# Optimization experiments

Hardware: AMD Instinct MI355X
Metric: run time of the kernel (lower is better)

## Reference

```python
import jax, jax.numpy as jnp
import numpy as np


def setup_inputs() -> dict:
    key = jax.random.key(0)
    ks = jax.random.split(key, 8)
    B, T, V, D, H, C = 1024, 80, 50000, 300, 300, 3
    sent = jax.random.randint(ks[0], (B, T), 0, V, dtype=jnp.int32)
    lens = jax.random.randint(ks[1], (B,), 1, T + 1, dtype=jnp.int32)
    emb = jax.random.normal(ks[2], (V, D), dtype=jnp.float32) * 0.1
    Wx = jax.random.normal(ks[3], (D, 4 * H), dtype=jnp.float32) * 0.05
    Wh = jax.random.normal(ks[4], (H, 4 * H), dtype=jnp.float32) * 0.05
    b = jnp.zeros((4 * H,), dtype=jnp.float32)
    Wout = jax.random.normal(ks[5], (H, C), dtype=jnp.float32) * 0.05
    bout = jnp.zeros((C,), dtype=jnp.float32)
    return {"sent": sent, "lens": lens, "emb": emb, "Wx": Wx, "Wh": Wh,
            "b": b, "Wout": Wout, "bout": bout}


def _lstm_masked(x, mask, Wx, Wh, b, H):
    # x: [B, T, D], mask: [B, T] float. Scan over time keeping h,c in carry.
    B = x.shape[0]
    h0 = jnp.zeros((B, H), dtype=x.dtype)
    c0 = jnp.zeros((B, H), dtype=x.dtype)

    def step(carry, inp):
        h, c = carry
        xt, mt = inp                      # xt: [B, D], mt: [B]
        gates = xt @ Wx + h @ Wh + b      # [B, 4H]
        i, f, g, o = jnp.split(gates, 4, axis=-1)
        i, f, o = jax.nn.sigmoid(i), jax.nn.sigmoid(f), jax.nn.sigmoid(o)
        g = jnp.tanh(g)
        c_new = f * c + i * g
        h_new = o * jnp.tanh(c_new)
        m = mt[:, None]
        h = m * h_new + (1.0 - m) * h     # mask-based state blending
        c = m * c_new + (1.0 - m) * c
        return (h, c), None

    xs = (jnp.swapaxes(x, 0, 1), jnp.swapaxes(mask, 0, 1))  # time-major
    (h, c), _ = jax.lax.scan(step, (h0, c0), xs)
    return h


def reference(sent, lens, emb, Wx, Wh, b, Wout, bout):
    T = sent.shape[1]
    H = Wh.shape[0]
    x = emb[sent]                                         # [B, T, D]
    mask = (jnp.arange(T)[None, :] < lens[:, None]).astype(x.dtype)  # [B, T]
    h = _lstm_masked(x, mask, Wx, Wh, b, H)
    logit = h @ Wout + bout                               # [B, C]
    return logit
```

## Files before the change

### kernel.cpp

```cpp
#include <hip/hip_runtime.h>
#include <hip/hip_fp16.h>


typedef float    f32x4 __attribute__((ext_vector_type(4)));
typedef _Float16 f16;
typedef _Float16 f16x8 __attribute__((ext_vector_type(8)));
typedef unsigned long long u64;

#define NB    1024
#define TT    80
#define NV    50000
#define ND    300
#define KP    320
#define NKT   10
#define SL    75
#define SLP   80
#define NTPG  5
#define NTIL  20
#define TPB   256
#define GRID  256
#define NSLAB 8

#define TAGMASK 0x0001000100010001ULL

#define OFF_EMB   0
#define OFF_WHP   32000000
#define OFF_WXP   32819200
#define OFF_HBUF  33638400
#define HBUF_SZ   (NB * KP)
#define OFF_HF32  38881280
#define WS_NEED   40110080

__global__ __launch_bounds__(256) void absa_prep_emb(
    const float* __restrict__ emb, f16* __restrict__ embb) {
  int i = blockIdx.x * 256 + threadIdx.x;
  if (i >= NV * KP / 8) return;
  int flat = i * 8;
  int row  = flat / KP;
  int k    = flat - row * KP;
  f16x8 o;
  if (k + 7 < ND) {
    float4 a = *reinterpret_cast<const float4*>(emb + row * ND + k);
    float4 b = *reinterpret_cast<const float4*>(emb + row * ND + k + 4);
    o[0] = (f16)a.x; o[1] = (f16)a.y; o[2] = (f16)a.z; o[3] = (f16)a.w;
    o[4] = (f16)b.x; o[5] = (f16)b.y; o[6] = (f16)b.z; o[7] = (f16)b.w;
  } else {
#pragma unroll
    for (int e = 0; e < 8; ++e) {
      int kk = k + e;
      float v = (kk < ND) ? emb[row * ND + kk] : (kk == ND ? 1.0f : 0.0f);
      o[e] = (f16)v;
    }
  }
  *reinterpret_cast<f16x8*>(embb + flat) = o;
}

__global__ __launch_bounds__(256) void absa_prep_pack2(
    const float* __restrict__ Wx, const float* __restrict__ Wh,
    const float* __restrict__ bias,
    f16* __restrict__ wxp, f16* __restrict__ whp) {
  const int half = 4 * NTIL * NKT * 512;
  int idx0 = blockIdx.x * 256 + threadIdx.x;
  if (idx0 >= 2 * half) return;
  int mode = idx0 >= half;
  int idx  = idx0 - mode * half;
  int e    = idx & 7;
  int lane = (idx >> 3) & 63;
  int fid  = idx >> 9;
  int kt   = fid % NKT;
  int rem  = fid / NKT;
  int nt   = rem % NTIL;
  int n    = rem / NTIL;
  int gi   = nt / NTPG, ti = nt - gi * NTPG;
  int k    = kt * 32 + (lane >> 4) * 8 + e;
  int cc   = ti * 16 + (lane & 15);
  float v = 0.f;
  if (cc < SL) {
    int col = gi * 300 + n * SL + cc;
    if (mode == 0) {
      if (k < ND)       v = Wx[k * 1200 + col];
      else if (k == ND) v = bias[col];
    } else {
      int kl = k % SLP, n2 = k / SLP;
      if (kl < SL)      v = Wh[(n2 * SL + kl) * 1200 + col];
    }
  }
  (mode ? whp : wxp)[idx] = (f16)v;
}

__device__ __forceinline__ float sigf(float x) {
  return __builtin_amdgcn_rcpf(1.f + __builtin_amdgcn_exp2f(-1.44269504f * x));
}
__device__ __forceinline__ float tanhf_(float x) {
  float xx = fminf(15.f, fmaxf(-15.f, x));
  return 1.f - 2.f * __builtin_amdgcn_rcpf(1.f + __builtin_amdgcn_exp2f(2.88539008f * xx));
}

__device__ __forceinline__ u64 tag_pat(int tg) {
  return ((u64)(tg & 1)) | ((u64)((tg >> 1) & 1) << 16) |
         ((u64)((tg >> 2) & 1) << 32) | ((u64)((tg >> 3) & 1) << 48);
}

__global__ __launch_bounds__(TPB, 1) void absa_lstm(
    const int* __restrict__ sent, const int* __restrict__ lens,
    const f16* __restrict__ embb,
    const f16* __restrict__ whp, const f16* __restrict__ wxp,
    f16* __restrict__ hbuf, float* __restrict__ hf32) {
  const int bid = blockIdx.x;
  const int s   = bid & 7;
  const int q   = bid >> 3;
  const int n   = q & 3;
  const int g   = s * 8 + (q >> 2);

  const int tid = threadIdx.x;
  const int w   = tid >> 6;
  const int l   = tid & 63;
  const int l15 = l & 15, lk = l >> 4;
  const int grow0 = g * 16;

  __shared__ float gates[2 * 4 * 80 * 20];
  __shared__ float c_lds[80 * 20];
  __shared__ float hf_lds[80 * 20];
  __shared__ int   sent_lds[16 * TT];
  __shared__ int   len_lds[16];

  for (int i = tid; i < 16 * TT; i += TPB) sent_lds[i] = sent[g * 16 * TT + i];
  if (tid < 16) len_lds[tid] = lens[grow0 + tid];
  for (int i = tid; i < 80 * 20; i += TPB) { c_lds[i] = 0.f; hf_lds[i] = 0.f; }
  __syncthreads();

  int maxlen = 0;
#pragma unroll
  for (int r = 0; r < 16; ++r) maxlen = max(maxlen, len_lds[r]);

  f16x8 wh[NTPG][NKT], wx[NTPG][NKT];
#pragma unroll
  for (int j = 0; j < NTPG; ++j)
#pragma unroll
    for (int kt = 0; kt < NKT; ++kt) {
      size_t off = ((size_t)(n * NTIL + (w * NTPG + j)) * NKT + kt) * 512 + l * 8;
      wh[j][kt] = *reinterpret_cast<const f16x8*>(whp + off);
      wx[j][kt] = *reinterpret_cast<const f16x8*>(wxp + off);
    }

  int gaddr[NTPG];
#pragma unroll
  for (int j = 0; j < NTPG; ++j)
    gaddr[j] = ((w * 80) + j * 16 + l15) * 20 + lk * 4;

  f32x4 acc[NTPG];

  auto xpart = [&](int t) {
#pragma unroll
    for (int j = 0; j < NTPG; ++j) acc[j] = (f32x4){0.f, 0.f, 0.f, 0.f};
    const int srow = sent_lds[l15 * TT + t];
    const f16* xb = embb + (size_t)srow * KP + lk * 8;
#pragma unroll
    for (int kt = 0; kt < NKT; ++kt) {
      f16x8 xa = *reinterpret_cast<const f16x8*>(xb + kt * 32);
#pragma unroll
      for (int j = 0; j < NTPG; ++j)
        acc[j] = __builtin_amdgcn_mfma_f32_16x16x32_f16(xa, wx[j][kt], acc[j], 0, 0, 0);
    }
  };

  xpart(0);

  for (int t = 0; t < maxlen; ++t) {
    const int par = (t & 1) * (4 * 80 * 20);

    if (t > 0) {
      const u64 expv = tag_pat((t - 1) % 15);
      const f16* hp = hbuf + (size_t)((t - 1) & 7) * HBUF_SZ + (grow0 + l15) * KP + lk * 8;
      u64 q0[NKT], q1[NKT];
#pragma unroll
      for (int kt = 0; kt < NKT; ++kt) {
        const u64* p = reinterpret_cast<const u64*>(hp + kt * 32);
        q0[kt] = __hip_atomic_load(p,     __ATOMIC_RELAXED, __HIP_MEMORY_SCOPE_AGENT);
        q1[kt] = __hip_atomic_load(p + 1, __ATOMIC_RELAXED, __HIP_MEMORY_SCOPE_AGENT);
      }
      bool any = true;
      int guard = 0;
      while (any && guard++ < (1 << 15)) {
        any = false;
#pragma unroll
        for (int kt = 0; kt < NKT; ++kt) {
          const u64* p = reinterpret_cast<const u64*>(hp + kt * 32);
          if ((q0[kt] & TAGMASK) != expv) {
            q0[kt] = __hip_atomic_load(p,     __ATOMIC_RELAXED, __HIP_MEMORY_SCOPE_AGENT);
            any = true;
          }
          if ((q1[kt] & TAGMASK) != expv) {
            q1[kt] = __hip_atomic_load(p + 1, __ATOMIC_RELAXED, __HIP_MEMORY_SCOPE_AGENT);
            any = true;
          }
        }
      }
#pragma unroll
      for (int kt = 0; kt < NKT; ++kt) {
        union { u64 qq[2]; f16x8 v; } u;
        u.qq[0] = q0[kt]; u.qq[1] = q1[kt];
#pragma unroll
        for (int j = 0; j < NTPG; ++j)
          acc[j] = __builtin_amdgcn_mfma_f32_16x16x32_f16(u.v, wh[j][kt], acc[j], 0, 0, 0);
      }
    }

#pragma unroll
    for (int j = 0; j < NTPG; ++j)
      *reinterpret_cast<f32x4*>(&gates[par + gaddr[j]]) = acc[j];
    __syncthreads();

    {
      const u64 pat = tag_pat(t % 15);
      f16* hc = hbuf + (size_t)(t & 7) * HBUF_SZ;
      for (int i = tid; i < 320; i += TPB) {
        int row = i & 15, qd = i >> 4;
        union { unsigned short us[4]; u64 uu; } pu;
#pragma unroll
        for (int e = 0; e < 4; ++e) {
          int cc = qd * 4 + e;
          float h = 0.f;
          if (cc < SL) {
            int base = cc * 20 + row;
            if (t < len_lds[row]) {
              float vi = gates[par + (0 * 80 + cc) * 20 + row];
              float vf = gates[par + (1 * 80 + cc) * 20 + row];
              float vg = gates[par + (2 * 80 + cc) * 20 + row];
              float vo = gates[par + (3 * 80 + cc) * 20 + row];
              float iv = sigf(vi), fv = sigf(vf), ov = sigf(vo);
              float gv = tanhf_(vg);
              float cn = fv * c_lds[base] + iv * gv;
              h = ov * tanhf_(cn);
              c_lds[base] = cn;
              hf_lds[base] = h;
            } else {
              h = hf_lds[base];
            }
          }
          union { f16 f; unsigned short u; } cv;
          cv.f = (f16)h;
          pu.us[e] = cv.u;
        }
        pu.uu = (pu.uu & ~TAGMASK) | pat;
        u64* dst = reinterpret_cast<u64*>(hc + (size_t)(grow0 + row) * KP + n * SLP + qd * 4);
        (void)__hip_atomic_exchange(dst, pu.uu, __ATOMIC_RELAXED, __HIP_MEMORY_SCOPE_AGENT);
      }
    }

    if (t + 1 < maxlen) xpart(t + 1);
  }

  __syncthreads();
  for (int i = tid; i < 16 * SL; i += TPB) {
    int row = i & 15, cc = i >> 4;
    hf32[(grow0 + row) * ND + n * SL + cc] = hf_lds[cc * 20 + row];
  }
}

__global__ __launch_bounds__(256) void absa_logits(
    const float* __restrict__ hf32, const float* __restrict__ Wout,
    const float* __restrict__ bout, float* __restrict__ out) {
  int row = blockIdx.x * 4 + (threadIdx.x >> 6);
  int l   = threadIdx.x & 63;
  float s0 = 0.f, s1 = 0.f, s2 = 0.f;
  for (int k = l; k < ND; k += 64) {
    float h  = hf32[row * ND + k];
    s0 += h * Wout[k * 3 + 0];
    s1 += h * Wout[k * 3 + 1];
    s2 += h * Wout[k * 3 + 2];
  }
#pragma unroll
  for (int o = 32; o; o >>= 1) {
    s0 += __shfl_down(s0, o);
    s1 += __shfl_down(s1, o);
    s2 += __shfl_down(s2, o);
  }
  if (l == 0) {
    out[row * 3 + 0] = s0 + bout[0];
    out[row * 3 + 1] = s1 + bout[1];
    out[row * 3 + 2] = s2 + bout[2];
  }
}

extern "C" void kernel_launch(void* const* d_in, const int* in_sizes, int n_in,
                              void* d_out, int out_size, void* d_ws, size_t ws_size,
                              hipStream_t stream) {
  const int*   sent = (const int*)d_in[0];
  const int*   lens = (const int*)d_in[1];
  const float* emb  = (const float*)d_in[2];
  const float* Wx   = (const float*)d_in[3];
  const float* Wh   = (const float*)d_in[4];
  const float* bv   = (const float*)d_in[5];
  const float* Wout = (const float*)d_in[6];
  const float* bout = (const float*)d_in[7];
  float* out = (float*)d_out;

  char* wsb = (char*)d_ws;
  f16*   embb = (f16*)(wsb + OFF_EMB);
  f16*   whp  = (f16*)(wsb + OFF_WHP);
  f16*   wxp  = (f16*)(wsb + OFF_WXP);
  f16*   hbuf = (f16*)(wsb + OFF_HBUF);
  float* hf32 = (float*)(wsb + OFF_HF32);

  (void)hipMemsetAsync(hbuf, 0xFF, NSLAB * NB * KP * 2, stream);

  absa_prep_emb  <<<(NV * KP / 8 + 255) / 256, 256, 0, stream>>>(emb, embb);
  absa_prep_pack2<<<2 * 4 * NTIL * NKT * 512 / 256, 256, 0, stream>>>(Wx, Wh, bv, wxp, whp);
  absa_lstm      <<<GRID, TPB, 0, stream>>>(sent, lens, embb, whp, wxp, hbuf, hf32);
  absa_logits    <<<NB / 4, 256, 0, stream>>>(hf32, Wout, bout, out);
}
```

Baseline: 685.5 us.

## Split LSTM recurrent GEMM K dimension across two wave groups per block

Doubles the block to 512 threads and splits the K dimension of the hidden-state and input matmuls across two groups of four waves. Each group writes its partial gate sums to a separate half of the gates buffer, and the elementwise pass adds the two halves. Each wave now keeps only half of the Wh fragments in registers. Wx is no longer held in registers and is reloaded from global memory on every step. The aim is to shorten each wave's serial MFMA chain and its polling of hbuf. The cost is more global traffic for Wx and a doubled gates buffer in LDS.

```diff
diff --git a/kernel.cpp b/kernel.cpp
--- a/kernel.cpp
+++ b/kernel.cpp
@@ -13,11 +13,12 @@
 #define ND    300
 #define KP    320
 #define NKT   10
+#define KTH   5
 #define SL    75
 #define SLP   80
 #define NTPG  5
 #define NTIL  20
-#define TPB   256
+#define TPB   512
 #define GRID  256
 #define NSLAB 8
 
@@ -101,24 +102,29 @@
          ((u64)((tg >> 2) & 1) << 32) | ((u64)((tg >> 3) & 1) << 48);
 }
 
-__global__ __launch_bounds__(TPB, 1) void absa_lstm(
+#define GSTRIDE (2 * 4 * 80 * 20)
+
+__global__ __launch_bounds__(TPB, 2) void absa_lstm(
     const int* __restrict__ sent, const int* __restrict__ lens,
     const f16* __restrict__ embb,
     const f16* __restrict__ whp, const f16* __restrict__ wxp,
     f16* __restrict__ hbuf, float* __restrict__ hf32) {
   const int bid = blockIdx.x;
   const int s   = bid & 7;
-  const int q   = bid >> 3;
-  const int n   = q & 3;
-  const int g   = s * 8 + (q >> 2);
-
-  const int tid = threadIdx.x;
-  const int w   = tid >> 6;
-  const int l   = tid & 63;
-  const int l15 = l & 15, lk = l >> 4;
+  const int qq  = bid >> 3;
+  const int n   = qq & 3;
+  const int g   = s * 8 + (qq >> 2);
+
+  const int tid  = threadIdx.x;
+  const int w    = tid >> 6;
+  const int gate = w & 3;
+  const int kh   = w >> 2;
+  const int kb   = kh * KTH;
+  const int l    = tid & 63;
+  const int l15  = l & 15, lk = l >> 4;
   const int grow0 = g * 16;
 
-  __shared__ float gates[2 * 4 * 80 * 20];
+  __shared__ float gates[2 * GSTRIDE];
   __shared__ float c_lds[80 * 20];
   __shared__ float hf_lds[80 * 20];
   __shared__ int   sent_lds[16 * TT];
@@ -133,20 +139,18 @@
 #pragma unroll
   for (int r = 0; r < 16; ++r) maxlen = max(maxlen, len_lds[r]);
 
-  f16x8 wh[NTPG][NKT], wx[NTPG][NKT];
+  f16x8 wh[NTPG][KTH];
 #pragma unroll
   for (int j = 0; j < NTPG; ++j)
 #pragma unroll
-    for (int kt = 0; kt < NKT; ++kt) {
-      size_t off = ((size_t)(n * NTIL + (w * NTPG + j)) * NKT + kt) * 512 + l * 8;
-      wh[j][kt] = *reinterpret_cast<const f16x8*>(whp + off);
-      wx[j][kt] = *reinterpret_cast<const f16x8*>(wxp + off);
-    }
+    for (int kk = 0; kk < KTH; ++kk)
+      wh[j][kk] = *reinterpret_cast<const f16x8*>(
+          whp + ((size_t)(n * NTIL + (gate * NTPG + j)) * NKT + (kb + kk)) * 512 + l * 8);
 
   int gaddr[NTPG];
 #pragma unroll
   for (int j = 0; j < NTPG; ++j)
-    gaddr[j] = ((w * 80) + j * 16 + l15) * 20 + lk * 4;
+    gaddr[j] = (((kh * 4 + gate) * 80) + j * 16 + l15) * 20 + lk * 4;
 
   f32x4 acc[NTPG];
 
@@ -156,53 +160,56 @@
     const int srow = sent_lds[l15 * TT + t];
     const f16* xb = embb + (size_t)srow * KP + lk * 8;
 #pragma unroll
-    for (int kt = 0; kt < NKT; ++kt) {
-      f16x8 xa = *reinterpret_cast<const f16x8*>(xb + kt * 32);
-#pragma unroll
-      for (int j = 0; j < NTPG; ++j)
-        acc[j] = __builtin_amdgcn_mfma_f32_16x16x32_f16(xa, wx[j][kt], acc[j], 0, 0, 0);
+    for (int kk = 0; kk < KTH; ++kk) {
+      f16x8 xa = *reinterpret_cast<const f16x8*>(xb + (kb + kk) * 32);
+#pragma unroll
+      for (int j = 0; j < NTPG; ++j) {
+        f16x8 wxf = *reinterpret_cast<const f16x8*>(
+            wxp + ((size_t)(n * NTIL + (gate * NTPG + j)) * NKT + (kb + kk)) * 512 + l * 8);
+        acc[j] = __builtin_amdgcn_mfma_f32_16x16x32_f16(xa, wxf, acc[j], 0, 0, 0);
+      }
     }
   };
 
   xpart(0);
 
   for (int t = 0; t < maxlen; ++t) {
-    const int par = (t & 1) * (4 * 80 * 20);
+    const int par = (t & 1) * GSTRIDE;
 
     if (t > 0) {
       const u64 expv = tag_pat((t - 1) % 15);
       const f16* hp = hbuf + (size_t)((t - 1) & 7) * HBUF_SZ + (grow0 + l15) * KP + lk * 8;
-      u64 q0[NKT], q1[NKT];
-#pragma unroll
-      for (int kt = 0; kt < NKT; ++kt) {
-        const u64* p = reinterpret_cast<const u64*>(hp + kt * 32);
-        q0[kt] = __hip_atomic_load(p,     __ATOMIC_RELAXED, __HIP_MEMORY_SCOPE_AGENT);
-        q1[kt] = __hip_atomic_load(p + 1, __ATOMIC_RELAXED, __HIP_MEMORY_SCOPE_AGENT);
+      u64 q0[KTH], q1[KTH];
+#pragma unroll
+      for (int kk = 0; kk < KTH; ++kk) {
+        const u64* p = reinterpret_cast<const u64*>(hp + (kb + kk) * 32);
+        q0[kk] = __hip_atomic_load(p,     __ATOMIC_RELAXED, __HIP_MEMORY_SCOPE_AGENT);
+        q1[kk] = __hip_atomic_load(p + 1, __ATOMIC_RELAXED, __HIP_MEMORY_SCOPE_AGENT);
       }
       bool any = true;
       int guard = 0;
       while (any && guard++ < (1 << 15)) {
         any = false;
 #pragma unroll
-        for (int kt = 0; kt < NKT; ++kt) {
-          const u64* p = reinterpret_cast<const u64*>(hp + kt * 32);
-          if ((q0[kt] & TAGMASK) != expv) {
-            q0[kt] = __hip_atomic_load(p,     __ATOMIC_RELAXED, __HIP_MEMORY_SCOPE_AGENT);
+        for (int kk = 0; kk < KTH; ++kk) {
+          const u64* p = reinterpret_cast<const u64*>(hp + (kb + kk) * 32);
+          if ((q0[kk] & TAGMASK) != expv) {
+            q0[kk] = __hip_atomic_load(p,     __ATOMIC_RELAXED, __HIP_MEMORY_SCOPE_AGENT);
             any = true;
           }
-          if ((q1[kt] & TAGMASK) != expv) {
-            q1[kt] = __hip_atomic_load(p + 1, __ATOMIC_RELAXED, __HIP_MEMORY_SCOPE_AGENT);
+          if ((q1[kk] & TAGMASK) != expv) {
+            q1[kk] = __hip_atomic_load(p + 1, __ATOMIC_RELAXED, __HIP_MEMORY_SCOPE_AGENT);
             any = true;
           }
         }
       }
 #pragma unroll
-      for (int kt = 0; kt < NKT; ++kt) {
-        union { u64 qq[2]; f16x8 v; } u;
-        u.qq[0] = q0[kt]; u.qq[1] = q1[kt];
+      for (int kk = 0; kk < KTH; ++kk) {
+        union { u64 qd[2]; f16x8 v; } u;
+        u.qd[0] = q0[kk]; u.qd[1] = q1[kk];
 #pragma unroll
         for (int j = 0; j < NTPG; ++j)
-          acc[j] = __builtin_amdgcn_mfma_f32_16x16x32_f16(u.v, wh[j][kt], acc[j], 0, 0, 0);
+          acc[j] = __builtin_amdgcn_mfma_f32_16x16x32_f16(u.v, wh[j][kk], acc[j], 0, 0, 0);
       }
     }
 
@@ -211,41 +218,39 @@
       *reinterpret_cast<f32x4*>(&gates[par + gaddr[j]]) = acc[j];
     __syncthreads();
 
-    {
+    if (tid < 320) {
       const u64 pat = tag_pat(t % 15);
       f16* hc = hbuf + (size_t)(t & 7) * HBUF_SZ;
-      for (int i = tid; i < 320; i += TPB) {
-        int row = i & 15, qd = i >> 4;
-        union { unsigned short us[4]; u64 uu; } pu;
-#pragma unroll
-        for (int e = 0; e < 4; ++e) {
-          int cc = qd * 4 + e;
-          float h = 0.f;
-          if (cc < SL) {
-            int base = cc * 20 + row;
-            if (t < len_lds[row]) {
-              float vi = gates[par + (0 * 80 + cc) * 20 + row];
-              float vf = gates[par + (1 * 80 + cc) * 20 + row];
-              float vg = gates[par + (2 * 80 + cc) * 20 + row];
-              float vo = gates[par + (3 * 80 + cc) * 20 + row];
-              float iv = sigf(vi), fv = sigf(vf), ov = sigf(vo);
-              float gv = tanhf_(vg);
-              float cn = fv * c_lds[base] + iv * gv;
-              h = ov * tanhf_(cn);
-              c_lds[base] = cn;
-              hf_lds[base] = h;
-            } else {
-              h = hf_lds[base];
-            }
+      int row = tid & 15, qd = tid >> 4;
+      union { unsigned short us[4]; u64 uu; } pu;
+#pragma unroll
+      for (int e = 0; e < 4; ++e) {
+        int cc = qd * 4 + e;
+        float h = 0.f;
+        if (cc < SL) {
+          int base = cc * 20 + row;
+          if (t < len_lds[row]) {
+            float vi = gates[par + ((0) * 80 + cc) * 20 + row] + gates[par + ((4 + 0) * 80 + cc) * 20 + row];
+            float vf = gates[par + ((1) * 80 + cc) * 20 + row] + gates[par + ((4 + 1) * 80 + cc) * 20 + row];
+            float vg = gates[par + ((2) * 80 + cc) * 20 + row] + gates[par + ((4 + 2) * 80 + cc) * 20 + row];
+            float vo = gates[par + ((3) * 80 + cc) * 20 + row] + gates[par + ((4 + 3) * 80 + cc) * 20 + row];
+            float iv = sigf(vi), fv = sigf(vf), ov = sigf(vo);
+            float gv = tanhf_(vg);
+            float cn = fv * c_lds[base] + iv * gv;
+            h = ov * tanhf_(cn);
+            c_lds[base] = cn;
+            hf_lds[base] = h;
+          } else {
+            h = hf_lds[base];
           }
-          union { f16 f; unsigned short u; } cv;
-          cv.f = (f16)h;
-          pu.us[e] = cv.u;
         }
-        pu.uu = (pu.uu & ~TAGMASK) | pat;
-        u64* dst = reinterpret_cast<u64*>(hc + (size_t)(grow0 + row) * KP + n * SLP + qd * 4);
-        (void)__hip_atomic_exchange(dst, pu.uu, __ATOMIC_RELAXED, __HIP_MEMORY_SCOPE_AGENT);
-      }
+        union { f16 f; unsigned short u; } cv;
+        cv.f = (f16)h;
+        pu.us[e] = cv.u;
+      }
+      pu.uu = (pu.uu & ~TAGMASK) | pat;
+      u64* dst = reinterpret_cast<u64*>(hc + (size_t)(grow0 + row) * KP + n * SLP + qd * 4);
+      (void)__hip_atomic_exchange(dst, pu.uu, __ATOMIC_RELAXED, __HIP_MEMORY_SCOPE_AGENT);
     }
 
     if (t + 1 < maxlen) xpart(t + 1);
```

New measurement: 1.181 ms. 72.3% more time.
